# Optimization experiments

Hardware: AMD Instinct MI355X
Metric: run time of the kernel (lower is better)

The kernel has to match this reference:

```python
import jax, jax.numpy as jnp
import numpy as np

B, S, D, H = 2, 2048, 1024, 16
DK = D // H

def setup_inputs() -> dict:
    key = jax.random.key(0)
    ks = jax.random.split(key, 8)
    def lin(k):
        kw, kb = jax.random.split(k)
        w = jax.random.normal(kw, (D, D), dtype=jnp.float32) / np.sqrt(D)
        b = jax.random.normal(kb, (D,), dtype=jnp.float32) * 0.01
        return w, b
    wq, bq = lin(ks[0]); wk, bk = lin(ks[1]); wv, bv = lin(ks[2]); wo, bo = lin(ks[3])
    return {
        'q': jax.random.normal(ks[4], (B, S, D), dtype=jnp.float32),
        'k': jax.random.normal(ks[5], (B, S, D), dtype=jnp.float32),
        'v': jax.random.normal(ks[6], (B, S, D), dtype=jnp.float32),
        'mask': jnp.ones((1, 1, S, S), dtype=jnp.int32),
        'wq': wq, 'bq': bq, 'wk': wk, 'bk': bk,
        'wv': wv, 'bv': bv, 'wo': wo, 'bo': bo,
    }

def reference(q, k, v, mask, wq, bq, wk, bk, wv, bv, wo, bo):
    b, s, _ = q.shape
    # QKV projections (nn.Linear: x @ W^T + b)
    Q = (q @ wq.T + bq).reshape(b, s, H, DK).transpose(0, 2, 1, 3)  # [B,H,S,DK]
    K = (k @ wk.T + bk).reshape(b, -1, H, DK).transpose(0, 2, 1, 3)
    V = (v @ wv.T + bv).reshape(b, -1, H, DK).transpose(0, 2, 1, 3)
    scores = jnp.einsum('bhqd,bhkd->bhqk', Q, K) / np.sqrt(DK)
    # faithful to source: masked positions set to -1e-09 (tiny, as written)
    scores = jnp.where(mask == 0, jnp.float32(-1e-09), scores)
    att = jax.nn.softmax(scores, axis=-1)
    x = jnp.einsum('bhqk,bhkd->bhqd', att, V)
    x = x.transpose(0, 2, 1, 3).reshape(b, s, H * DK)
    return x @ wo.T + bo
```

## Files before the change

kernel.cpp:

```cpp
#include <hip/hip_runtime.h>
#include <stdint.h>

typedef unsigned short u16;
typedef unsigned int u32;
typedef __bf16 bf16x8 __attribute__((ext_vector_type(8)));
typedef __bf16 bf16x2 __attribute__((ext_vector_type(2)));
typedef float f32x4 __attribute__((ext_vector_type(4)));
typedef float f32x16 __attribute__((ext_vector_type(16)));
typedef unsigned short u16x4 __attribute__((ext_vector_type(4)));
typedef unsigned short u16x8 __attribute__((ext_vector_type(8)));
typedef u32 u32x4 __attribute__((ext_vector_type(4)));

#define B_ 2
#define S_ 2048
#define D_ 1024
#define H_ 16

__device__ __forceinline__ u16 f2bf(float f) {
  uint32_t u = __builtin_bit_cast(uint32_t, f);
  u += 0x7FFF + ((u >> 16) & 1);
  return (u16)(u >> 16);
}

__device__ __forceinline__ u32 pkbf(float x, float y) {
  bf16x2 t;
  t.x = (__bf16)x;
  t.y = (__bf16)y;
  return __builtin_bit_cast(u32, t);
}

__device__ __forceinline__ void pl32swap(u32& a, u32& b) {
  asm("v_permlane32_swap_b32 %0, %1" : "+v"(a), "+v"(b));
}

__device__ __forceinline__ void gld_lds16(const void* g, void* l) {
  __builtin_amdgcn_global_load_lds((const __attribute__((address_space(1))) void*)g,
                                   (__attribute__((address_space(3))) void*)l, 16, 0, 0);
}

__global__ void cvt_all(const float* __restrict__ q, const float* __restrict__ k,
                        const float* __restrict__ v, const float* __restrict__ wq,
                        const float* __restrict__ wk, const float* __restrict__ wv,
                        const float* __restrict__ wo, u16* __restrict__ qb,
                        u16* __restrict__ kb, u16* __restrict__ vb, u16* __restrict__ wqb,
                        u16* __restrict__ wkb, u16* __restrict__ wvb, u16* __restrict__ wob) {
  int bid = blockIdx.x;
  const float* s;
  u16* d;
  int base;
  if (bid < 4096)       { s = q;  d = qb;  base = bid; }
  else if (bid < 8192)  { s = k;  d = kb;  base = bid - 4096; }
  else if (bid < 12288) { s = v;  d = vb;  base = bid - 8192; }
  else if (bid < 13312) { s = wq; d = wqb; base = bid - 12288; }
  else if (bid < 14336) { s = wk; d = wkb; base = bid - 13312; }
  else if (bid < 15360) { s = wv; d = wvb; base = bid - 14336; }
  else                  { s = wo; d = wob; base = bid - 15360; }
  int i = (base * 256 + threadIdx.x) * 4;
  float4 f = *(const float4*)(s + i);
  u16x4 o;
  o.x = f2bf(f.x); o.y = f2bf(f.y); o.z = f2bf(f.z); o.w = f2bf(f.w);
  *(u16x4*)(d + i) = o;
}

template <int EPI>
__device__ __forceinline__ void gemm_body(const u16* __restrict__ A, const u16* __restrict__ W,
                                          const float* __restrict__ bias, void* __restrict__ Cp,
                                          float scale) {
  constexpr int K = 1024;
  constexpr int N = 1024;
  __shared__ __align__(16) u16 As[128 * 64];
  __shared__ __align__(16) u16 Ws[128 * 64];
  const int tid = threadIdx.x;
  const int lane = tid & 63, wid = tid >> 6;
  const int wm = wid >> 1, wn = wid & 1;
  const int l15 = lane & 15, l4 = lane >> 4;
  const int m0 = blockIdx.y * 128, n0 = blockIdx.x * 128;

  f32x4 acc[4][4] = {};

  for (int kt = 0; kt < K / 64; ++kt) {
    __syncthreads();
#pragma unroll
    for (int i = 0; i < 4; ++i) {
      int c = i * 256 + tid;
      int row = c >> 3;
      int scb = ((c & 7) << 4) ^ ((row & 7) << 4);
      size_t goff = (size_t)kt * 64 + (scb >> 1);
      gld_lds16(A + (size_t)(m0 + row) * K + goff, (char*)As + (size_t)c * 16);
      gld_lds16(W + (size_t)(n0 + row) * K + goff, (char*)Ws + (size_t)c * 16);
    }
    __syncthreads();
#pragma unroll
    for (int kk = 0; kk < 2; ++kk) {
      bf16x8 af[4], bfr[4];
#pragma unroll
      for (int m = 0; m < 4; ++m) {
        int row = wm * 64 + m * 16 + l15;
        int cb = (kk * 64 + l4 * 16) ^ ((row & 7) << 4);
        af[m] = *(const bf16x8*)((const char*)As + row * 128 + cb);
      }
#pragma unroll
      for (int n = 0; n < 4; ++n) {
        int row = wn * 64 + n * 16 + l15;
        int cb = (kk * 64 + l4 * 16) ^ ((row & 7) << 4);
        bfr[n] = *(const bf16x8*)((const char*)Ws + row * 128 + cb);
      }
#pragma unroll
      for (int m = 0; m < 4; ++m)
#pragma unroll
        for (int n = 0; n < 4; ++n)
          acc[m][n] = __builtin_amdgcn_mfma_f32_16x16x32_bf16(af[m], bfr[n], acc[m][n], 0, 0, 0);
    }
  }

  if (EPI == 0) {
    float* C = (float*)Cp;
#pragma unroll
    for (int m = 0; m < 4; ++m)
#pragma unroll
      for (int n = 0; n < 4; ++n) {
        int col = n0 + wn * 64 + n * 16 + l15;
        float bval = bias[col];
#pragma unroll
        for (int j = 0; j < 4; ++j) {
          int r = m0 + wm * 64 + m * 16 + l4 * 4 + j;
          C[(size_t)r * N + col] = acc[m][n][j] + bval;
        }
      }
  } else if (EPI == 1) {
    u16* C = (u16*)Cp;
#pragma unroll
    for (int m = 0; m < 4; ++m)
#pragma unroll
      for (int n = 0; n < 4; ++n) {
        int col = n0 + wn * 64 + n * 16 + l15;
        float bval = bias[col];
        int h = col >> 6, dk = col & 63;
#pragma unroll
        for (int j = 0; j < 4; ++j) {
          int r = m0 + wm * 64 + m * 16 + l4 * 4 + j;
          int bb = r >> 11, s = r & 2047;
          C[(((size_t)bb * H_ + h) * S_ + s) * 64 + dk] = f2bf((acc[m][n][j] + bval) * scale);
        }
      }
  } else {
    u16* C = (u16*)Cp;
#pragma unroll
    for (int m = 0; m < 4; ++m)
#pragma unroll
      for (int n = 0; n < 4; ++n) {
        int col = n0 + wn * 64 + n * 16 + l15;
        float bval = bias[col];
        int h = col >> 6, dk = col & 63;
        int r0 = m0 + wm * 64 + m * 16 + l4 * 4;
        int bb = r0 >> 11, s0 = r0 & 2047;
        u16x4 o;
#pragma unroll
        for (int j = 0; j < 4; ++j) o[j] = f2bf(acc[m][n][j] + bval);
        *(u16x4*)(C + (((size_t)bb * H_ + h) * 64 + dk) * S_ + s0) = o;
      }
  }
}

__global__ __launch_bounds__(256) void gemm_qkv(
    const u16* __restrict__ qb, const u16* __restrict__ kb, const u16* __restrict__ vb,
    const u16* __restrict__ wqb, const u16* __restrict__ wkb, const u16* __restrict__ wvb,
    const float* __restrict__ bq, const float* __restrict__ bk, const float* __restrict__ bv,
    u16* __restrict__ Qp, u16* __restrict__ Kp, u16* __restrict__ VTp) {
  int z = blockIdx.z;
  if (z == 2) {
    gemm_body<2>(vb, wvb, bv, VTp, 1.0f);
  } else if (z == 1) {
    gemm_body<1>(kb, wkb, bk, Kp, 1.0f);
  } else {
    gemm_body<1>(qb, wqb, bq, Qp, 0.1803368801111244f);
  }
}

__global__ __launch_bounds__(256) void gemm_out(
    const u16* __restrict__ xb, const u16* __restrict__ wob,
    const float* __restrict__ bo, float* __restrict__ out) {
  gemm_body<0>(xb, wob, bo, out, 1.0f);
}

__global__ __launch_bounds__(256, 2) void attn(
    const u16* __restrict__ Qp, const u16* __restrict__ Kp,
    const u16* __restrict__ VTp, u16* __restrict__ xb) {
  const int flat = blockIdx.x;
  const int nf = (flat & 7) * 64 + (flat >> 3);
  const int bh = nf >> 4, qt = nf & 15;
  const int b = bh >> 4, h = bh & 15;
  const size_t kbase = (size_t)bh * S_ * 64;
  const int tid = threadIdx.x, lane = tid & 63, w = tid >> 6;
  const int l31 = lane & 31, hi = lane >> 5;

  __shared__ __align__(16) u16 Ks[2][64 * 64];
  __shared__ __align__(16) u16 Vs[2][64 * 64];

  bf16x8 qf[4];
  {
    const u16* qrow = Qp + kbase + (size_t)(qt * 128 + w * 32 + l31) * 64;
#pragma unroll
    for (int kk = 0; kk < 4; ++kk)
      qf[kk] = *(const bf16x8*)(qrow + kk * 16 + hi * 8);
  }

  float m = -1e30f, lsum = 0.f;
  f32x16 xacc[2] = {};

  auto stage = [&](int bi, int t) {
#pragma unroll
    for (int i = 0; i < 2; ++i) {
      int c = i * 256 + tid;
      int row = c >> 3;
      int scb = (((c & 7) ^ (row & 7) ^ ((row >> 3) & 3)) << 4);
      gld_lds16(Kp + kbase + (size_t)(t * 64 + row) * 64 + (scb >> 1),
                (char*)Ks[bi] + (size_t)c * 16);
    }
#pragma unroll
    for (int i = 0; i < 2; ++i) {
      int c = i * 256 + tid;
      int row = c >> 3;
      int scb = (((c & 7) ^ (row & 7) ^ ((row >> 3) & 3)) << 4);
      gld_lds16(VTp + kbase + (size_t)row * S_ + t * 64 + (scb >> 1),
                (char*)Vs[bi] + (size_t)c * 16);
    }
  };

  stage(0, 0);
  for (int t = 0; t < S_ / 64; ++t) {
    const int cur = t & 1;
    __syncthreads();
    if (t + 1 < S_ / 64) stage(cur ^ 1, t + 1);

    const u16* Kb = Ks[cur];
    const u16* Vb = Vs[cur];

    f32x16 sacc[2] = {};
    __builtin_amdgcn_s_setprio(1);
#pragma unroll
    for (int kk = 0; kk < 4; ++kk)
#pragma unroll
      for (int kvt = 0; kvt < 2; ++kvt) {
        int row = kvt * 32 + l31;
        int cb = (kk * 32 + hi * 16) ^ ((((row & 7) ^ ((row >> 3) & 3))) << 4);
        bf16x8 kf = *(const bf16x8*)((const char*)Kb + row * 128 + cb);
        sacc[kvt] = __builtin_amdgcn_mfma_f32_32x32x16_bf16(kf, qf[kk], sacc[kvt], 0, 0, 0);
      }
    __builtin_amdgcn_s_setprio(0);

    float mx;
    {
      float a = fmaxf(fmaxf(sacc[0][0], sacc[0][1]), fmaxf(sacc[0][2], sacc[0][3]));
      float b2 = fmaxf(fmaxf(sacc[0][4], sacc[0][5]), fmaxf(sacc[0][6], sacc[0][7]));
      float c = fmaxf(fmaxf(sacc[0][8], sacc[0][9]), fmaxf(sacc[0][10], sacc[0][11]));
      float d = fmaxf(fmaxf(sacc[0][12], sacc[0][13]), fmaxf(sacc[0][14], sacc[0][15]));
      float e = fmaxf(fmaxf(sacc[1][0], sacc[1][1]), fmaxf(sacc[1][2], sacc[1][3]));
      float f = fmaxf(fmaxf(sacc[1][4], sacc[1][5]), fmaxf(sacc[1][6], sacc[1][7]));
      float g = fmaxf(fmaxf(sacc[1][8], sacc[1][9]), fmaxf(sacc[1][10], sacc[1][11]));
      float h2 = fmaxf(fmaxf(sacc[1][12], sacc[1][13]), fmaxf(sacc[1][14], sacc[1][15]));
      float x = fmaxf(fmaxf(a, b2), fmaxf(c, d));
      float y = fmaxf(fmaxf(e, f), fmaxf(g, h2));
      x = fmaxf(x, y);
      mx = fmaxf(x, __shfl_xor(x, 32, 64));
    }

    if (__any(mx - m > 8.f)) {
      float nm = fmaxf(m, mx);
      float sc = __builtin_amdgcn_exp2f(m - nm);
      m = nm;
      lsum *= sc;
#pragma unroll
      for (int r = 0; r < 16; ++r) {
        int src = ((r & 3) + 8 * (r >> 2) + 4 * hi) | (hi << 5);
        float f = __shfl(sc, src, 64);
        xacc[0][r] *= f;
        xacc[1][r] *= f;
      }
    }

    float p[2][16];
    float sum = 0.f;
#pragma unroll
    for (int t2 = 0; t2 < 2; ++t2)
#pragma unroll
      for (int r = 0; r < 16; ++r) {
        float e = __builtin_amdgcn_exp2f(sacc[t2][r] - m);
        p[t2][r] = e;
        sum += e;
      }
    sum += __shfl_xor(sum, 32, 64);
    lsum += sum;

#pragma unroll
    for (int kk = 0; kk < 4; ++kk) {
      const int t2 = kk >> 1, rb = (kk & 1) * 8;
      u32 a0 = pkbf(p[t2][rb + 0], p[t2][rb + 1]);
      u32 a1 = pkbf(p[t2][rb + 2], p[t2][rb + 3]);
      u32 b0 = pkbf(p[t2][rb + 4], p[t2][rb + 5]);
      u32 b1 = pkbf(p[t2][rb + 6], p[t2][rb + 7]);
      pl32swap(a0, b0);
      pl32swap(a1, b1);
      u32x4 wv;
      wv.x = a0; wv.y = a1; wv.z = b0; wv.w = b1;
      bf16x8 pf = __builtin_bit_cast(bf16x8, wv);
      __builtin_amdgcn_s_setprio(1);
#pragma unroll
      for (int dn = 0; dn < 2; ++dn) {
        int row = dn * 32 + l31;
        int cb = (kk * 32 + hi * 16) ^ ((((row & 7) ^ ((row >> 3) & 3))) << 4);
        bf16x8 vf = *(const bf16x8*)((const char*)Vb + row * 128 + cb);
        xacc[dn] = __builtin_amdgcn_mfma_f32_32x32x16_bf16(pf, vf, xacc[dn], 0, 0, 0);
      }
      __builtin_amdgcn_s_setprio(0);
    }
  }

  float linv = 1.f / lsum;
#pragma unroll
  for (int r = 0; r < 16; ++r) {
    int qr = (r & 3) + 8 * (r >> 2) + 4 * hi;
    float f = __shfl(linv, qr | (hi << 5), 64);
    int qg = qt * 128 + w * 32 + qr;
    size_t rowb = ((size_t)b * S_ + qg) * D_ + h * 64;
    xb[rowb + l31] = f2bf(xacc[0][r] * f);
    xb[rowb + 32 + l31] = f2bf(xacc[1][r] * f);
  }
}

extern "C" void kernel_launch(void* const* d_in, const int* in_sizes, int n_in,
                              void* d_out, int out_size, void* d_ws, size_t ws_size,
                              hipStream_t stream) {
  const float* q  = (const float*)d_in[0];
  const float* k  = (const float*)d_in[1];
  const float* v  = (const float*)d_in[2];
  const float* wq = (const float*)d_in[4];
  const float* bq = (const float*)d_in[5];
  const float* wk = (const float*)d_in[6];
  const float* bk = (const float*)d_in[7];
  const float* wv = (const float*)d_in[8];
  const float* bv = (const float*)d_in[9];
  const float* wo = (const float*)d_in[10];
  const float* bo = (const float*)d_in[11];
  float* out = (float*)d_out;

  char* ws = (char*)d_ws;
  const size_t MB = 1u << 20;
  u16* qb  = (u16*)(ws + 0 * MB);
  u16* kb  = (u16*)(ws + 8 * MB);
  u16* vb  = (u16*)(ws + 16 * MB);
  u16* wqb = (u16*)(ws + 24 * MB);
  u16* wkb = (u16*)(ws + 26 * MB);
  u16* wvb = (u16*)(ws + 28 * MB);
  u16* wob = (u16*)(ws + 30 * MB);
  u16* Qp  = (u16*)(ws + 32 * MB);
  u16* Kp  = (u16*)(ws + 40 * MB);
  u16* VTp = (u16*)(ws + 48 * MB);
  u16* xb  = (u16*)(ws + 56 * MB);

  cvt_all<<<16384, 256, 0, stream>>>(q, k, v, wq, wk, wv, wo,
                                     qb, kb, vb, wqb, wkb, wvb, wob);
  gemm_qkv<<<dim3(8, 32, 3), 256, 0, stream>>>(qb, kb, vb, wqb, wkb, wvb,
                                               bq, bk, bv, Qp, Kp, VTp);
  attn<<<512, 256, 0, stream>>>(Qp, Kp, VTp, xb);
  gemm_out<<<dim3(8, 32), 256, 0, stream>>>(xb, wob, bo, out);
}
```

Baseline: 141.7 us.

## Fuse fp32-to-bf16 activation conversion into QKV GEMM and narrow output GEMM tile

The separate conversion pass over the q/k/v activations is removed. The QKV GEMM now reads fp32 activations directly, prefetching the next K-tile into registers and converting to bf16 while writing into LDS. This saves the extra write and re-read of about 24MB of bf16 activations, at the cost of more registers and a synchronous register-to-LDS store instead of direct global-to-LDS loads. The output GEMM uses a 64-wide N tile, doubling its grid to 512 blocks for better CU coverage.

```diff
diff --git a/kernel.cpp b/kernel.cpp
--- a/kernel.cpp
+++ b/kernel.cpp
@@ -38,23 +38,18 @@
                                    (__attribute__((address_space(3))) void*)l, 16, 0, 0);
 }
 
-__global__ void cvt_all(const float* __restrict__ q, const float* __restrict__ k,
-                        const float* __restrict__ v, const float* __restrict__ wq,
-                        const float* __restrict__ wk, const float* __restrict__ wv,
-                        const float* __restrict__ wo, u16* __restrict__ qb,
-                        u16* __restrict__ kb, u16* __restrict__ vb, u16* __restrict__ wqb,
-                        u16* __restrict__ wkb, u16* __restrict__ wvb, u16* __restrict__ wob) {
+__global__ void cvt_w(const float* __restrict__ wq, const float* __restrict__ wk,
+                      const float* __restrict__ wv, const float* __restrict__ wo,
+                      u16* __restrict__ wqb, u16* __restrict__ wkb,
+                      u16* __restrict__ wvb, u16* __restrict__ wob) {
   int bid = blockIdx.x;
   const float* s;
   u16* d;
   int base;
-  if (bid < 4096)       { s = q;  d = qb;  base = bid; }
-  else if (bid < 8192)  { s = k;  d = kb;  base = bid - 4096; }
-  else if (bid < 12288) { s = v;  d = vb;  base = bid - 8192; }
-  else if (bid < 13312) { s = wq; d = wqb; base = bid - 12288; }
-  else if (bid < 14336) { s = wk; d = wkb; base = bid - 13312; }
-  else if (bid < 15360) { s = wv; d = wvb; base = bid - 14336; }
-  else                  { s = wo; d = wob; base = bid - 15360; }
+  if (bid < 1024)       { s = wq; d = wqb; base = bid; }
+  else if (bid < 2048)  { s = wk; d = wkb; base = bid - 1024; }
+  else if (bid < 3072)  { s = wv; d = wvb; base = bid - 2048; }
+  else                  { s = wo; d = wob; base = bid - 3072; }
   int i = (base * 256 + threadIdx.x) * 4;
   float4 f = *(const float4*)(s + i);
   u16x4 o;
@@ -62,37 +57,80 @@
   *(u16x4*)(d + i) = o;
 }
 
-template <int EPI>
-__device__ __forceinline__ void gemm_body(const u16* __restrict__ A, const u16* __restrict__ W,
+template <int EPI, bool A_FP32, int BN>
+__device__ __forceinline__ void gemm_body(const void* __restrict__ Ap, const u16* __restrict__ W,
                                           const float* __restrict__ bias, void* __restrict__ Cp,
                                           float scale) {
   constexpr int K = 1024;
   constexpr int N = 1024;
+  constexpr int NFR = BN / 32;
   __shared__ __align__(16) u16 As[128 * 64];
-  __shared__ __align__(16) u16 Ws[128 * 64];
+  __shared__ __align__(16) u16 Ws[BN * 64];
   const int tid = threadIdx.x;
   const int lane = tid & 63, wid = tid >> 6;
   const int wm = wid >> 1, wn = wid & 1;
   const int l15 = lane & 15, l4 = lane >> 4;
-  const int m0 = blockIdx.y * 128, n0 = blockIdx.x * 128;
-
-  f32x4 acc[4][4] = {};
-
+  const int m0 = blockIdx.y * 128, n0 = blockIdx.x * BN;
+
+  f32x4 acc[4][NFR] = {};
+
+  float4 areg[8];
+  auto loadA = [&](int kt) {
+    if (A_FP32) {
+      const float* Af = (const float*)Ap;
+#pragma unroll
+      for (int i = 0; i < 4; ++i) {
+        int c = i * 256 + tid;
+        int row = c >> 3, col8 = c & 7;
+        const float* src = Af + (size_t)(m0 + row) * K + kt * 64 + col8 * 8;
+        areg[2 * i]     = *(const float4*)(src);
+        areg[2 * i + 1] = *(const float4*)(src + 4);
+      }
+    }
+  };
+  auto writeA = [&]() {
+#pragma unroll
+    for (int i = 0; i < 4; ++i) {
+      int c = i * 256 + tid;
+      int row = c >> 3, col8 = c & 7;
+      u16x8 o;
+      o[0] = f2bf(areg[2 * i].x);     o[1] = f2bf(areg[2 * i].y);
+      o[2] = f2bf(areg[2 * i].z);     o[3] = f2bf(areg[2 * i].w);
+      o[4] = f2bf(areg[2 * i + 1].x); o[5] = f2bf(areg[2 * i + 1].y);
+      o[6] = f2bf(areg[2 * i + 1].z); o[7] = f2bf(areg[2 * i + 1].w);
+      *(u16x8*)((char*)As + row * 128 + ((col8 << 4) ^ ((row & 7) << 4))) = o;
+    }
+  };
+
+  loadA(0);
   for (int kt = 0; kt < K / 64; ++kt) {
     __syncthreads();
-#pragma unroll
-    for (int i = 0; i < 4; ++i) {
+    if (A_FP32) {
+      writeA();
+    } else {
+      const u16* Ab = (const u16*)Ap;
+#pragma unroll
+      for (int i = 0; i < 4; ++i) {
+        int c = i * 256 + tid;
+        int row = c >> 3;
+        int scb = ((c & 7) << 4) ^ ((row & 7) << 4);
+        gld_lds16(Ab + (size_t)(m0 + row) * K + (size_t)kt * 64 + (scb >> 1),
+                  (char*)As + (size_t)c * 16);
+      }
+    }
+#pragma unroll
+    for (int i = 0; i < BN / 32; ++i) {
       int c = i * 256 + tid;
       int row = c >> 3;
       int scb = ((c & 7) << 4) ^ ((row & 7) << 4);
-      size_t goff = (size_t)kt * 64 + (scb >> 1);
-      gld_lds16(A + (size_t)(m0 + row) * K + goff, (char*)As + (size_t)c * 16);
-      gld_lds16(W + (size_t)(n0 + row) * K + goff, (char*)Ws + (size_t)c * 16);
-    }
+      gld_lds16(W + (size_t)(n0 + row) * K + (size_t)kt * 64 + (scb >> 1),
+                (char*)Ws + (size_t)c * 16);
+    }
+    if (kt + 1 < K / 64) loadA(kt + 1);
     __syncthreads();
 #pragma unroll
     for (int kk = 0; kk < 2; ++kk) {
-      bf16x8 af[4], bfr[4];
+      bf16x8 af[4], bfr[NFR];
 #pragma unroll
       for (int m = 0; m < 4; ++m) {
         int row = wm * 64 + m * 16 + l15;
@@ -100,15 +138,15 @@
         af[m] = *(const bf16x8*)((const char*)As + row * 128 + cb);
       }
 #pragma unroll
-      for (int n = 0; n < 4; ++n) {
-        int row = wn * 64 + n * 16 + l15;
+      for (int n = 0; n < NFR; ++n) {
+        int row = wn * (BN / 2) + n * 16 + l15;
         int cb = (kk * 64 + l4 * 16) ^ ((row & 7) << 4);
         bfr[n] = *(const bf16x8*)((const char*)Ws + row * 128 + cb);
       }
 #pragma unroll
       for (int m = 0; m < 4; ++m)
 #pragma unroll
-        for (int n = 0; n < 4; ++n)
+        for (int n = 0; n < NFR; ++n)
           acc[m][n] = __builtin_amdgcn_mfma_f32_16x16x32_bf16(af[m], bfr[n], acc[m][n], 0, 0, 0);
     }
   }
@@ -118,8 +156,8 @@
 #pragma unroll
     for (int m = 0; m < 4; ++m)
 #pragma unroll
-      for (int n = 0; n < 4; ++n) {
-        int col = n0 + wn * 64 + n * 16 + l15;
+      for (int n = 0; n < NFR; ++n) {
+        int col = n0 + wn * (BN / 2) + n * 16 + l15;
         float bval = bias[col];
 #pragma unroll
         for (int j = 0; j < 4; ++j) {
@@ -132,8 +170,8 @@
 #pragma unroll
     for (int m = 0; m < 4; ++m)
 #pragma unroll
-      for (int n = 0; n < 4; ++n) {
-        int col = n0 + wn * 64 + n * 16 + l15;
+      for (int n = 0; n < NFR; ++n) {
+        int col = n0 + wn * (BN / 2) + n * 16 + l15;
         float bval = bias[col];
         int h = col >> 6, dk = col & 63;
 #pragma unroll
@@ -148,8 +186,8 @@
 #pragma unroll
     for (int m = 0; m < 4; ++m)
 #pragma unroll
-      for (int n = 0; n < 4; ++n) {
-        int col = n0 + wn * 64 + n * 16 + l15;
+      for (int n = 0; n < NFR; ++n) {
+        int col = n0 + wn * (BN / 2) + n * 16 + l15;
         float bval = bias[col];
         int h = col >> 6, dk = col & 63;
         int r0 = m0 + wm * 64 + m * 16 + l4 * 4;
@@ -163,24 +201,24 @@
 }
 
 __global__ __launch_bounds__(256) void gemm_qkv(
-    const u16* __restrict__ qb, const u16* __restrict__ kb, const u16* __restrict__ vb,
+    const float* __restrict__ q, const float* __restrict__ k, const float* __restrict__ v,
     const u16* __restrict__ wqb, const u16* __restrict__ wkb, const u16* __restrict__ wvb,
     const float* __restrict__ bq, const float* __restrict__ bk, const float* __restrict__ bv,
     u16* __restrict__ Qp, u16* __restrict__ Kp, u16* __restrict__ VTp) {
   int z = blockIdx.z;
   if (z == 2) {
-    gemm_body<2>(vb, wvb, bv, VTp, 1.0f);
+    gemm_body<2, true, 128>(v, wvb, bv, VTp, 1.0f);
   } else if (z == 1) {
-    gemm_body<1>(kb, wkb, bk, Kp, 1.0f);
+    gemm_body<1, true, 128>(k, wkb, bk, Kp, 1.0f);
   } else {
-    gemm_body<1>(qb, wqb, bq, Qp, 0.1803368801111244f);
+    gemm_body<1, true, 128>(q, wqb, bq, Qp, 0.1803368801111244f);
   }
 }
 
 __global__ __launch_bounds__(256) void gemm_out(
     const u16* __restrict__ xb, const u16* __restrict__ wob,
     const float* __restrict__ bo, float* __restrict__ out) {
-  gemm_body<0>(xb, wob, bo, out, 1.0f);
+  gemm_body<0, false, 64>(xb, wob, bo, out, 1.0f);
 }
 
 __global__ __launch_bounds__(256, 2) void attn(
@@ -346,22 +384,18 @@
 
   char* ws = (char*)d_ws;
   const size_t MB = 1u << 20;
-  u16* qb  = (u16*)(ws + 0 * MB);
-  u16* kb  = (u16*)(ws + 8 * MB);
-  u16* vb  = (u16*)(ws + 16 * MB);
-  u16* wqb = (u16*)(ws + 24 * MB);
-  u16* wkb = (u16*)(ws + 26 * MB);
-  u16* wvb = (u16*)(ws + 28 * MB);
-  u16* wob = (u16*)(ws + 30 * MB);
-  u16* Qp  = (u16*)(ws + 32 * MB);
-  u16* Kp  = (u16*)(ws + 40 * MB);
-  u16* VTp = (u16*)(ws + 48 * MB);
-  u16* xb  = (u16*)(ws + 56 * MB);
-
-  cvt_all<<<16384, 256, 0, stream>>>(q, k, v, wq, wk, wv, wo,
-                                     qb, kb, vb, wqb, wkb, wvb, wob);
-  gemm_qkv<<<dim3(8, 32, 3), 256, 0, stream>>>(qb, kb, vb, wqb, wkb, wvb,
+  u16* wqb = (u16*)(ws + 0 * MB);
+  u16* wkb = (u16*)(ws + 2 * MB);
+  u16* wvb = (u16*)(ws + 4 * MB);
+  u16* wob = (u16*)(ws + 6 * MB);
+  u16* Qp  = (u16*)(ws + 8 * MB);
+  u16* Kp  = (u16*)(ws + 16 * MB);
+  u16* VTp = (u16*)(ws + 24 * MB);
+  u16* xb  = (u16*)(ws + 32 * MB);
+
+  cvt_w<<<4096, 256, 0, stream>>>(wq, wk, wv, wo, wqb, wkb, wvb, wob);
+  gemm_qkv<<<dim3(8, 32, 3), 256, 0, stream>>>(q, k, v, wqb, wkb, wvb,
                                                bq, bk, bv, Qp, Kp, VTp);
   attn<<<512, 256, 0, stream>>>(Qp, Kp, VTp, xb);
-  gemm_out<<<dim3(8, 32), 256, 0, stream>>>(xb, wob, bo, out);
-}
+  gemm_out<<<dim3(16, 32), 256, 0, stream>>>(xb, wob, bo, out);
+}
```

Measured after the change: 151.8 us. +7.1%, slower.
